# Performance work log

Measured on AMD Instinct MI355X. Metric: run time of the kernel, lower is better.

Reference implementation:

```python
import jax, jax.numpy as jnp
import numpy as np

B, N, D, DEPTH = 1, 512, 128, 4


def mlp_apply(W, x):
    # W: (depth, d, d), x: (..., d). First layer has no activation, then silu before each matmul.
    x = x @ W[0]
    for i in range(1, DEPTH):
        x = jax.nn.silu(x) @ W[i]
    return x


def _binop(x, y):
    # linear recurrence combine: s_t = a_t * s_{t-1} + b_t
    a1, b1 = x
    a2, b2 = y
    return (a1 * a2, a2 * b1 + b2)


def setup_inputs() -> dict:
    key = jax.random.key(0)
    ks = jax.random.split(key, 7)
    s = 0.02  # scale for projection weights (torch Linear-like init magnitude)
    return {
        "seq": jax.random.normal(ks[0], (B, N, D), jnp.float32),
        "W_mem": jax.random.normal(ks[1], (DEPTH, D, D), jnp.float32) * (D ** -0.5),
        "W_q": jax.random.normal(ks[2], (D, D), jnp.float32) * s,
        "W_kv": jax.random.normal(ks[3], (D, 2 * D), jnp.float32) * s,
        "W_mom": jax.random.normal(ks[4], (D, 1), jnp.float32) * s,
        "W_step": jax.random.normal(ks[5], (D, 1), jnp.float32) * s,
        "W_decay": jax.random.normal(ks[6], (D, 1), jnp.float32) * s,
    }


def reference(seq, W_mem, W_q, W_kv, W_mom, W_step, W_decay):
    b, n, d = seq.shape
    # --- store_memories ---
    adaptive_lr = (seq @ W_step)[..., 0]            # (b, n)
    adaptive_mom = seq @ W_mom                      # (b, n, 1)
    decay = jax.nn.sigmoid(seq @ W_decay)           # (b, n, 1)

    kv = seq.reshape(b * n, d) @ W_kv               # (bn, 2d)
    keys, values = kv[:, :d], kv[:, d:]

    def loss_fn(W, k, v):
        pred = mlp_apply(W, k)                      # (d,)
        # (pred - v)^2 .mean(-1).sum() for a single sample == mean over d
        return jnp.mean((pred - v) ** 2)

    # per-sample meta-gradients wrt memory MLP weights
    losses, grads = jax.vmap(jax.value_and_grad(loss_fn, argnums=0), in_axes=(None, 0, 0))(W_mem, keys, values)
    grads = grads.reshape(b, n, DEPTH, d, d)
    surprise = grads * (-adaptive_lr)[..., None, None, None]   # (b,n,depth,d,d)

    # momentum_t = adaptive_mom_t * momentum_{t-1} + surprise_t  (assoc. scan over n)
    am = adaptive_mom[..., None, None]              # (b, n, 1, 1, 1)
    _, momentum = jax.lax.associative_scan(_binop, (am, surprise), axis=1)

    # update_t = (1 - decay_t) * update_{t-1} + momentum_t
    dec = (1.0 - decay)[..., None, None]            # (b, n, 1, 1, 1)
    _, updates = jax.lax.associative_scan(_binop, (dec, momentum), axis=1)

    # --- retrieve_memories with per-token updated weights ---
    q = (seq @ W_q).reshape(b * n, d)
    W_tok = (W_mem[None, None] + updates).reshape(b * n, DEPTH, d, d)
    retrieved = jax.vmap(mlp_apply)(W_tok, q).reshape(b, n, d)
    return retrieved
```

## Files before the change

kernel.cpp:

```cpp
#include <hip/hip_runtime.h>
#include <hip/hip_bf16.h>
#include <math.h>

#define N 512
#define NN (N*N)
#define D 128
#define DD (D*D)
#define ND (N*D)
#define LSTR 132
#define CSTR 68

__device__ __forceinline__ float sigmoidf_(float x) { return 1.f / (1.f + expf(-x)); }

__global__ void k_transpose(const float* __restrict__ W_mem, float* __restrict__ WT) {
    int idx = blockIdx.x * 256 + threadIdx.x;
    int l = idx / DD;
    int r = idx % DD;
    int i = r / D;
    int j = r % D;
    WT[idx] = W_mem[(l + 1) * DD + j * D + i];
}

__global__ __launch_bounds__(512) void k_phase1(
    const float* __restrict__ seq, const float* __restrict__ W_mem,
    const float* __restrict__ W_q, const float* __restrict__ W_kv,
    const float* __restrict__ W_mom, const float* __restrict__ W_step,
    const float* __restrict__ W_decay, const float* __restrict__ WT,
    float* __restrict__ Q, float* __restrict__ INS, float* __restrict__ ES,
    float* __restrict__ am, float* __restrict__ dec)
{
    __shared__ float s_seq[D], s_v[D], s_cur[D];
    __shared__ float s_h[4][D];
    __shared__ float s_part[4][D];
    __shared__ float s_p3[4][3][D];
    __shared__ float s_red[8];
    __shared__ float s_lr;

    const int t = blockIdx.x;
    const int tid = threadIdx.x;
    const int j = tid & 127;
    const int p = tid >> 7;
    const int i0 = p * 32;

    if (p == 0) s_seq[j] = seq[t * D + j];
    __syncthreads();

    float ps = 0.f;
    if (p == 1) ps = s_seq[j] * W_step[j];
    else if (p == 2) ps = s_seq[j] * W_mom[j];
    else if (p == 3) ps = s_seq[j] * W_decay[j];
#pragma unroll
    for (int off = 32; off > 0; off >>= 1) ps += __shfl_down(ps, off);
    if ((tid & 63) == 0) s_red[tid >> 6] = ps;
    __syncthreads();
    if (tid == 0) s_lr = s_red[2] + s_red[3];
    else if (tid == 1) am[t] = s_red[4] + s_red[5];
    else if (tid == 2) dec[t] = 1.f - sigmoidf_(s_red[6] + s_red[7]);

    float kp = 0.f, vp = 0.f, qp = 0.f;
#pragma unroll 8
    for (int ii = 0; ii < 32; ii++) {
        int i = i0 + ii;
        float si = s_seq[i];
        kp += si * W_kv[i * 256 + j];
        vp += si * W_kv[i * 256 + 128 + j];
        qp += si * W_q[i * 128 + j];
    }
    s_p3[p][0][j] = kp; s_p3[p][1][j] = vp; s_p3[p][2][j] = qp;
    __syncthreads();
    if (p == 0) {
        float kj = s_p3[0][0][j] + s_p3[1][0][j] + s_p3[2][0][j] + s_p3[3][0][j];
        s_cur[j] = kj;
        INS[t * D + j] = kj;
    } else if (p == 1) {
        s_v[j] = s_p3[0][1][j] + s_p3[1][1][j] + s_p3[2][1][j] + s_p3[3][1][j];
    } else if (p == 2) {
        Q[t * D + j] = s_p3[0][2][j] + s_p3[1][2][j] + s_p3[2][2][j] + s_p3[3][2][j];
    }
    __syncthreads();

    for (int l = 0; l < 4; l++) {
        const float* Wl = W_mem + l * DD;
        float yp = 0.f;
#pragma unroll 8
        for (int ii = 0; ii < 32; ii++) {
            int i = i0 + ii;
            yp += s_cur[i] * Wl[i * D + j];
        }
        s_part[p][j] = yp;
        __syncthreads();
        if (p == 0) {
            float y = s_part[0][j] + s_part[1][j] + s_part[2][j] + s_part[3][j];
            s_h[l][j] = y;
            if (l < 3) {
                float a = y * sigmoidf_(y);
                s_cur[j] = a;
                INS[(l + 1) * ND + t * D + j] = a;
            }
        }
        __syncthreads();
    }

    if (p == 0) {
        float e = -s_lr * (2.f / (float)D) * (s_h[3][j] - s_v[j]);
        ES[3 * ND + t * D + j] = e;
        s_cur[j] = e;
    }
    __syncthreads();

    for (int l = 3; l >= 1; l--) {
        const float* Wt = WT + (l - 1) * DD;
        float gp = 0.f;
#pragma unroll 8
        for (int ii = 0; ii < 32; ii++) {
            int i = i0 + ii;
            gp += s_cur[i] * Wt[i * D + j];
        }
        s_part[p][j] = gp;
        __syncthreads();
        if (p == 0) {
            float g = s_part[0][j] + s_part[1][j] + s_part[2][j] + s_part[3][j];
            float h = s_h[l - 1][j];
            float sg = sigmoidf_(h);
            float e2 = g * (sg * (1.f + h * (1.f - sg)));
            ES[(l - 1) * ND + t * D + j] = e2;
            s_cur[j] = e2;
        }
        __syncthreads();
    }
}

__global__ __launch_bounds__(512) void k_logscan(
    const float* __restrict__ am, const float* __restrict__ dec,
    double* __restrict__ LA, double* __restrict__ LDp, int* __restrict__ NC)
{
    __shared__ double sa[N], sd[N];
    __shared__ int sn[N];
    const int t = threadIdx.x;
    float a = am[t];
    float d = dec[t];
    sa[t] = log((double)fmaxf(fabsf(a), 1e-38f));
    sd[t] = log((double)fmaxf(d, 1e-38f));
    sn[t] = (a < 0.f) ? 1 : 0;
    __syncthreads();
    for (int off = 1; off < N; off <<= 1) {
        double va = 0.0, vd = 0.0; int vn = 0;
        if (t >= off) { va = sa[t - off]; vd = sd[t - off]; vn = sn[t - off]; }
        __syncthreads();
        sa[t] += va; sd[t] += vd; sn[t] += vn;
        __syncthreads();
    }
    LA[t] = sa[t]; LDp[t] = sd[t]; NC[t] = sn[t];
}

__global__ __launch_bounds__(256) void k_build(
    const double* __restrict__ LA, const double* __restrict__ LDp,
    const int* __restrict__ NC,
    float* __restrict__ Amat, float* __restrict__ Dmat)
{
    int idx = blockIdx.x * 256 + threadIdx.x;
    int u = idx >> 9;
    int s = idx & (N - 1);
    float va = 0.f, vd = 0.f;
    if (s <= u) {
        va = expf((float)(LA[u] - LA[s]));
        if ((NC[u] - NC[s]) & 1) va = -va;
        vd = expf((float)(LDp[u] - LDp[s]));
    }
    Amat[idx] = va;
    Dmat[idx] = vd;
}

__global__ __launch_bounds__(256) void k_betamm(
    const float* __restrict__ Dmat, const float* __restrict__ Amat,
    float* __restrict__ betaP)
{
    const int bs = blockIdx.x;
    const int bt = blockIdx.y;
    const int z  = blockIdx.z;
    if (bs > bt) return;
    const int span = bt - bs + 1;
    const int chunk = (span + 3) >> 2;
    const int kBeg = bs + z * chunk;
    const int kEnd = (kBeg + chunk < bt + 1) ? (kBeg + chunk) : (bt + 1);
    if (kBeg >= kEnd) return;

    __shared__ float sA[32 * 34];
    __shared__ float sDT[32 * 34];

    const int tid = threadIdx.x;
    const int tx = tid & 15;
    const int ty = tid >> 4;
    float acc00 = 0.f, acc01 = 0.f, acc10 = 0.f, acc11 = 0.f;

    for (int kt = kBeg; kt < kEnd; kt++) {
        for (int i = tid; i < 1024; i += 256) {
            int r = i >> 5, c = i & 31;
            sA[r * 34 + c]  = Amat[(kt * 32 + r) * N + bs * 32 + c];
            sDT[c * 34 + r] = Dmat[(bt * 32 + r) * N + kt * 32 + c];
        }
        __syncthreads();
#pragma unroll 8
        for (int k = 0; k < 32; k++) {
            float2 a = *(float2*)&sA[k * 34 + 2 * tx];
            float2 d = *(float2*)&sDT[k * 34 + 2 * ty];
            acc00 += d.x * a.x; acc01 += d.x * a.y;
            acc10 += d.y * a.x; acc11 += d.y * a.y;
        }
        __syncthreads();
    }
    float* bp = betaP + z * NN + (bt * 32 + 2 * ty) * N + bs * 32 + 2 * tx;
    *(float2*)bp       = make_float2(acc00, acc01);
    *(float2*)(bp + N) = make_float2(acc10, acc11);
}

__global__ __launch_bounds__(256) void k_betared(
    const float* __restrict__ betaP, float* __restrict__ beta)
{
    int idx4 = blockIdx.x * 256 + threadIdx.x;
    int t  = idx4 >> 7;
    int s0 = (idx4 & 127) * 4;
    int bt = t >> 5, bs = s0 >> 5;
    float4 v = make_float4(0.f, 0.f, 0.f, 0.f);
    if (bs <= bt) {
        int span = bt - bs + 1;
        int chunk = (span + 3) >> 2;
        int nz = (span + chunk - 1) / chunk;
        v = *(const float4*)(betaP + t * N + s0);
        for (int z = 1; z < nz; z++) {
            float4 u = *(const float4*)(betaP + z * NN + t * N + s0);
            v.x += u.x; v.y += u.y; v.z += u.z; v.w += u.w;
        }
    }
    *(float4*)(beta + t * N + s0) = v;
}

__global__ __launch_bounds__(256) void k_layer(
    const float* __restrict__ Xsrc, float* __restrict__ Pout,
    const float* __restrict__ Wl, const float* __restrict__ INSl,
    const float* __restrict__ ESl, const float* __restrict__ beta,
    int mode)
{
    const int r = blockIdx.x;
    const int z = blockIdx.y;
    const bool isW = (z == 8);
    if (!isW && 4 * z > r) return;
    const int t0 = r * 16;
    const int lane = threadIdx.x;

    __shared__ __align__(16) float sX[16 * LSTR];
    __shared__ __align__(16) float sI[64 * LSTR];
    __shared__ __align__(16) float sE[32 * LSTR];
    __shared__ __align__(16) float sc[16 * CSTR];

    const int nzs = (r >> 2) + 1;
#pragma unroll
    for (int i = 0; i < 2; i++) {
        int f4 = lane + 256 * i;
        int row = f4 >> 5, c4 = f4 & 31;
        float4 v = ((const float4*)(Xsrc + t0 * D))[f4];
        if (mode) {
            for (int zz = 1; zz < nzs; zz++) {
                float4 u = ((const float4*)(Xsrc + zz * ND + t0 * D))[f4];
                v.x += u.x; v.y += u.y; v.z += u.z; v.w += u.w;
            }
            float4 w = ((const float4*)(Xsrc + 8 * ND + t0 * D))[f4];
            v.x += w.x; v.y += w.y; v.z += w.z; v.w += w.w;
            v.x = v.x * sigmoidf_(v.x); v.y = v.y * sigmoidf_(v.y);
            v.z = v.z * sigmoidf_(v.z); v.w = v.w * sigmoidf_(v.w);
        }
        *(float4*)(sX + row * LSTR + c4 * 4) = v;
    }

    if (isW) {
        __syncthreads();
        const int ti  = lane >> 4;
        const int j8  = (lane & 15) * 8;
        float acc[8];
#pragma unroll
        for (int b = 0; b < 8; b++) acc[b] = 0.f;
#pragma unroll 4
        for (int k = 0; k < D; k++) {
            float4 w0 = *(const float4*)(Wl + k * D + j8);
            float4 w1 = *(const float4*)(Wl + k * D + j8 + 4);
            float xv = sX[ti * LSTR + k];
            acc[0] += xv * w0.x; acc[1] += xv * w0.y;
            acc[2] += xv * w0.z; acc[3] += xv * w0.w;
            acc[4] += xv * w1.x; acc[5] += xv * w1.y;
            acc[6] += xv * w1.z; acc[7] += xv * w1.w;
        }
        float* yp = Pout + 8 * ND + (t0 + ti) * D + j8;
        *(float4*)yp       = make_float4(acc[0], acc[1], acc[2], acc[3]);
        *(float4*)(yp + 4) = make_float4(acc[4], acc[5], acc[6], acc[7]);
        return;
    }

    const int s0 = z * 64;

#pragma unroll
    for (int i = 0; i < 8; i++) {
        int f4 = lane + 256 * i;
        int row = f4 >> 5, c4 = f4 & 31;
        float4 a = ((const float4*)(INSl + s0 * D))[f4];
        *(float4*)(sI + row * LSTR + c4 * 4) = a;
    }

    const int rp = lane >> 5;
    const int sp = lane & 31;
    float b00 = beta[(t0 + 2 * rp) * N + s0 + sp];
    float b01 = beta[(t0 + 2 * rp) * N + s0 + sp + 32];
    float b10 = beta[(t0 + 2 * rp + 1) * N + s0 + sp];
    float b11 = beta[(t0 + 2 * rp + 1) * N + s0 + sp + 32];
    __syncthreads();

    float g00 = 0.f, g01 = 0.f, g10 = 0.f, g11 = 0.f;
#pragma unroll 8
    for (int k4 = 0; k4 < D; k4 += 4) {
        float4 a0 = *(float4*)(sX + (2 * rp) * LSTR + k4);
        float4 a1 = *(float4*)(sX + (2 * rp + 1) * LSTR + k4);
        float4 p0 = *(float4*)(sI + sp * LSTR + k4);
        float4 p1 = *(float4*)(sI + (sp + 32) * LSTR + k4);
        g00 += a0.x * p0.x + a0.y * p0.y + a0.z * p0.z + a0.w * p0.w;
        g01 += a0.x * p1.x + a0.y * p1.y + a0.z * p1.z + a0.w * p1.w;
        g10 += a1.x * p0.x + a1.y * p0.y + a1.z * p0.z + a1.w * p0.w;
        g11 += a1.x * p1.x + a1.y * p1.y + a1.z * p1.z + a1.w * p1.w;
    }
    sc[(2 * rp) * CSTR + sp]          = g00 * b00;
    sc[(2 * rp) * CSTR + sp + 32]     = g01 * b01;
    sc[(2 * rp + 1) * CSTR + sp]      = g10 * b10;
    sc[(2 * rp + 1) * CSTR + sp + 32] = g11 * b11;

    const int tp = lane >> 5;
    const int jc = (lane & 31) * 4;
    float acc[2][4];
#pragma unroll
    for (int a = 0; a < 2; a++)
#pragma unroll
        for (int b = 0; b < 4; b++) acc[a][b] = 0.f;

    for (int sub = 0; sub < 2; sub++) {
        __syncthreads();
#pragma unroll
        for (int i = 0; i < 4; i++) {
            int f4 = lane + 256 * i;
            int row = f4 >> 5, c4 = f4 & 31;
            float4 b = ((const float4*)(ESl + (s0 + sub * 32) * D))[f4];
            *(float4*)(sE + row * LSTR + c4 * 4) = b;
        }
        __syncthreads();
        const float* scp0 = sc + tp * CSTR + sub * 32;
        const float* scp1 = sc + (tp + 8) * CSTR + sub * 32;
#pragma unroll 8
        for (int s = 0; s < 32; s++) {
            float c0 = scp0[s];
            float c1 = scp1[s];
            float4 e = *(float4*)(sE + s * LSTR + jc);
            acc[0][0] += c0 * e.x; acc[0][1] += c0 * e.y;
            acc[0][2] += c0 * e.z; acc[0][3] += c0 * e.w;
            acc[1][0] += c1 * e.x; acc[1][1] += c1 * e.y;
            acc[1][2] += c1 * e.z; acc[1][3] += c1 * e.w;
        }
    }

    float* yp0 = Pout + z * ND + (t0 + tp) * D + jc;
    float* yp1 = Pout + z * ND + (t0 + tp + 8) * D + jc;
    *(float4*)yp0 = make_float4(acc[0][0], acc[0][1], acc[0][2], acc[0][3]);
    *(float4*)yp1 = make_float4(acc[1][0], acc[1][1], acc[1][2], acc[1][3]);
}

__global__ __launch_bounds__(256) void k_reduce(
    const float* __restrict__ P, float* __restrict__ out)
{
    int f4 = blockIdx.x * 256 + threadIdx.x;
    int t = f4 >> 5;
    int r = t >> 4;
    int nzs = (r >> 2) + 1;
    float4 v = ((const float4*)P)[f4];
    for (int zz = 1; zz < nzs; zz++) {
        float4 u = ((const float4*)(P + zz * ND))[f4];
        v.x += u.x; v.y += u.y; v.z += u.z; v.w += u.w;
    }
    float4 w = ((const float4*)(P + 8 * ND))[f4];
    v.x += w.x; v.y += w.y; v.z += w.z; v.w += w.w;
    ((float4*)out)[f4] = v;
}

extern "C" void kernel_launch(void* const* d_in, const int* in_sizes, int n_in,
                              void* d_out, int out_size, void* d_ws, size_t ws_size,
                              hipStream_t stream) {
    const float* seq     = (const float*)d_in[0];
    const float* W_mem   = (const float*)d_in[1];
    const float* W_q     = (const float*)d_in[2];
    const float* W_kv    = (const float*)d_in[3];
    const float* W_mom   = (const float*)d_in[4];
    const float* W_step  = (const float*)d_in[5];
    const float* W_decay = (const float*)d_in[6];
    float* out = (float*)d_out;

    float* ws   = (float*)d_ws;
    float* am   = ws;
    float* dec  = am + N;
    float* Q    = dec + N;
    float* INS  = Q + ND;
    float* ES   = INS + 4 * ND;
    float* beta = ES + 4 * ND;
    float* WT   = beta + NN;
    float* Amat = WT + 3 * DD;
    float* Dmat = Amat + NN;
    float* Pa   = Dmat + NN;
    float* Pb   = Pa + 9 * ND;
    double* LA  = (double*)(Pb + 9 * ND);
    double* LDp = LA + N;
    int* NC     = (int*)(LDp + N);
    float* betaP = Pa;

    k_transpose<<<192, 256, 0, stream>>>(W_mem, WT);
    k_phase1<<<N, 512, 0, stream>>>(seq, W_mem, W_q, W_kv, W_mom, W_step, W_decay,
                                    WT, Q, INS, ES, am, dec);
    k_logscan<<<1, N, 0, stream>>>(am, dec, LA, LDp, NC);
    k_build<<<(NN) / 256, 256, 0, stream>>>(LA, LDp, NC, Amat, Dmat);
    dim3 mmgrid(N / 32, N / 32, 4);
    k_betamm<<<mmgrid, 256, 0, stream>>>(Dmat, Amat, betaP);
    k_betared<<<NN / 4 / 256, 256, 0, stream>>>(betaP, beta);

    dim3 lgrid(32, 9);
    k_layer<<<lgrid, 256, 0, stream>>>(Q,  Pa, W_mem,          INS,          ES,          beta, 0);
    k_layer<<<lgrid, 256, 0, stream>>>(Pa, Pb, W_mem + DD,     INS + ND,     ES + ND,     beta, 1);
    k_layer<<<lgrid, 256, 0, stream>>>(Pb, Pa, W_mem + 2 * DD, INS + 2 * ND, ES + 2 * ND, beta, 1);
    k_layer<<<lgrid, 256, 0, stream>>>(Pa, Pb, W_mem + 3 * DD, INS + 3 * ND, ES + 3 * ND, beta, 1);
    k_reduce<<<64, 256, 0, stream>>>(Pb, out);
}
```

Measured before the change: 163.2 us.

## Process four tokens per block in phase1 with one token per 128-thread group

Restructures k_phase1 so each 512-thread block handles four tokens, with each 128-thread group owning one token and each thread computing a full 128-length dot product. This replaces the old split-K across four thread groups, dropping the shared-memory partial-sum reductions and the extra barriers. Hidden activations move into registers. In exchange each thread runs a longer serial loop, and the grid shrinks to 128 blocks, which may underfill the GPU's compute units, while loads of the shared weights are now shared by four tokens per block.

Result: slower. 172.5 us (+5.7%).

```diff
diff --git a/kernel.cpp b/kernel.cpp
--- a/kernel.cpp
+++ b/kernel.cpp
@@ -29,104 +29,111 @@
     float* __restrict__ Q, float* __restrict__ INS, float* __restrict__ ES,
     float* __restrict__ am, float* __restrict__ dec)
 {
-    __shared__ float s_seq[D], s_v[D], s_cur[D];
-    __shared__ float s_h[4][D];
-    __shared__ float s_part[4][D];
-    __shared__ float s_p3[4][3][D];
-    __shared__ float s_red[8];
-    __shared__ float s_lr;
-
-    const int t = blockIdx.x;
+    __shared__ float s_seq[4][D];
+    __shared__ float s_bufA[4][D];
+    __shared__ float s_bufB[4][D];
+    __shared__ float s_red[4][2][3];
+    __shared__ float s_lr[4];
+
     const int tid = threadIdx.x;
-    const int j = tid & 127;
-    const int p = tid >> 7;
-    const int i0 = p * 32;
-
-    if (p == 0) s_seq[j] = seq[t * D + j];
+    const int tok = tid >> 7;
+    const int j   = tid & 127;
+    const int t   = blockIdx.x * 4 + tok;
+
+    float sv = seq[t * D + j];
+    s_seq[tok][j] = sv;
+
+    float p0 = sv * W_step[j];
+    float p1 = sv * W_mom[j];
+    float p2 = sv * W_decay[j];
+#pragma unroll
+    for (int off = 32; off > 0; off >>= 1) {
+        p0 += __shfl_down(p0, off);
+        p1 += __shfl_down(p1, off);
+        p2 += __shfl_down(p2, off);
+    }
+    if ((tid & 63) == 0) {
+        int w = (tid >> 6) & 1;
+        s_red[tok][w][0] = p0;
+        s_red[tok][w][1] = p1;
+        s_red[tok][w][2] = p2;
+    }
     __syncthreads();
-
-    float ps = 0.f;
-    if (p == 1) ps = s_seq[j] * W_step[j];
-    else if (p == 2) ps = s_seq[j] * W_mom[j];
-    else if (p == 3) ps = s_seq[j] * W_decay[j];
-#pragma unroll
-    for (int off = 32; off > 0; off >>= 1) ps += __shfl_down(ps, off);
-    if ((tid & 63) == 0) s_red[tid >> 6] = ps;
+    if (j == 0) {
+        s_lr[tok] = s_red[tok][0][0] + s_red[tok][1][0];
+        am[t]     = s_red[tok][0][1] + s_red[tok][1][1];
+        dec[t]    = 1.f - sigmoidf_(s_red[tok][0][2] + s_red[tok][1][2]);
+    }
+
+    float kj = 0.f, vj = 0.f, qj = 0.f;
+    {
+        const float* sq = s_seq[tok];
+#pragma unroll 8
+        for (int i = 0; i < D; i++) {
+            float si = sq[i];
+            kj += si * W_kv[i * 256 + j];
+            vj += si * W_kv[i * 256 + 128 + j];
+            qj += si * W_q[i * 128 + j];
+        }
+    }
+    Q[t * D + j] = qj;
+    INS[t * D + j] = kj;
+    s_bufA[tok][j] = kj;
     __syncthreads();
-    if (tid == 0) s_lr = s_red[2] + s_red[3];
-    else if (tid == 1) am[t] = s_red[4] + s_red[5];
-    else if (tid == 2) dec[t] = 1.f - sigmoidf_(s_red[6] + s_red[7]);
-
-    float kp = 0.f, vp = 0.f, qp = 0.f;
-#pragma unroll 8
-    for (int ii = 0; ii < 32; ii++) {
-        int i = i0 + ii;
-        float si = s_seq[i];
-        kp += si * W_kv[i * 256 + j];
-        vp += si * W_kv[i * 256 + 128 + j];
-        qp += si * W_q[i * 128 + j];
-    }
-    s_p3[p][0][j] = kp; s_p3[p][1][j] = vp; s_p3[p][2][j] = qp;
-    __syncthreads();
-    if (p == 0) {
-        float kj = s_p3[0][0][j] + s_p3[1][0][j] + s_p3[2][0][j] + s_p3[3][0][j];
-        s_cur[j] = kj;
-        INS[t * D + j] = kj;
-    } else if (p == 1) {
-        s_v[j] = s_p3[0][1][j] + s_p3[1][1][j] + s_p3[2][1][j] + s_p3[3][1][j];
-    } else if (p == 2) {
-        Q[t * D + j] = s_p3[0][2][j] + s_p3[1][2][j] + s_p3[2][2][j] + s_p3[3][2][j];
-    }
-    __syncthreads();
-
-    for (int l = 0; l < 4; l++) {
-        const float* Wl = W_mem + l * DD;
-        float yp = 0.f;
-#pragma unroll 8
-        for (int ii = 0; ii < 32; ii++) {
-            int i = i0 + ii;
-            yp += s_cur[i] * Wl[i * D + j];
-        }
-        s_part[p][j] = yp;
-        __syncthreads();
-        if (p == 0) {
-            float y = s_part[0][j] + s_part[1][j] + s_part[2][j] + s_part[3][j];
-            s_h[l][j] = y;
+
+    float hreg[4];
+    float pred = 0.f;
+    {
+        float* curs[2] = { &s_bufA[0][0], &s_bufB[0][0] };
+        for (int l = 0; l < 4; l++) {
+            const float* cur = curs[l & 1] + tok * D;
+            float* nxt = curs[(l + 1) & 1] + tok * D;
+            const float* Wp = W_mem + l * DD + j;
+            float a0 = 0.f, a1 = 0.f, a2 = 0.f, a3 = 0.f;
+#pragma unroll 8
+            for (int i = 0; i < D; i += 4) {
+                a0 += cur[i]     * Wp[i * D];
+                a1 += cur[i + 1] * Wp[(i + 1) * D];
+                a2 += cur[i + 2] * Wp[(i + 2) * D];
+                a3 += cur[i + 3] * Wp[(i + 3) * D];
+            }
+            float y = (a0 + a1) + (a2 + a3);
+            hreg[l] = y;
             if (l < 3) {
                 float a = y * sigmoidf_(y);
-                s_cur[j] = a;
+                nxt[j] = a;
                 INS[(l + 1) * ND + t * D + j] = a;
+            } else {
+                pred = y;
             }
-        }
-        __syncthreads();
-    }
-
-    if (p == 0) {
-        float e = -s_lr * (2.f / (float)D) * (s_h[3][j] - s_v[j]);
+            __syncthreads();
+        }
+
+        float e = -s_lr[tok] * (2.f / (float)D) * (pred - vj);
         ES[3 * ND + t * D + j] = e;
-        s_cur[j] = e;
-    }
-    __syncthreads();
-
-    for (int l = 3; l >= 1; l--) {
-        const float* Wt = WT + (l - 1) * DD;
-        float gp = 0.f;
-#pragma unroll 8
-        for (int ii = 0; ii < 32; ii++) {
-            int i = i0 + ii;
-            gp += s_cur[i] * Wt[i * D + j];
-        }
-        s_part[p][j] = gp;
-        __syncthreads();
-        if (p == 0) {
-            float g = s_part[0][j] + s_part[1][j] + s_part[2][j] + s_part[3][j];
-            float h = s_h[l - 1][j];
+        curs[0][tok * D + j] = e;
+        __syncthreads();
+
+        for (int l = 3; l >= 1; l--) {
+            const float* cur = curs[(3 - l) & 1] + tok * D;
+            float* nxt = curs[(3 - l + 1) & 1] + tok * D;
+            const float* Wp = WT + (l - 1) * DD + j;
+            float a0 = 0.f, a1 = 0.f, a2 = 0.f, a3 = 0.f;
+#pragma unroll 8
+            for (int i = 0; i < D; i += 4) {
+                a0 += cur[i]     * Wp[i * D];
+                a1 += cur[i + 1] * Wp[(i + 1) * D];
+                a2 += cur[i + 2] * Wp[(i + 2) * D];
+                a3 += cur[i + 3] * Wp[(i + 3) * D];
+            }
+            float g = (a0 + a1) + (a2 + a3);
+            float h = hreg[l - 1];
             float sg = sigmoidf_(h);
             float e2 = g * (sg * (1.f + h * (1.f - sg)));
             ES[(l - 1) * ND + t * D + j] = e2;
-            s_cur[j] = e2;
-        }
-        __syncthreads();
+            nxt[j] = e2;
+            __syncthreads();
+        }
     }
 }
 
@@ -296,7 +303,6 @@
     }
 
     const int s0 = z * 64;
-
 #pragma unroll
     for (int i = 0; i < 8; i++) {
         int f4 = lane + 256 * i;
@@ -415,8 +421,8 @@
     float* betaP = Pa;
 
     k_transpose<<<192, 256, 0, stream>>>(W_mem, WT);
-    k_phase1<<<N, 512, 0, stream>>>(seq, W_mem, W_q, W_kv, W_mom, W_step, W_decay,
-                                    WT, Q, INS, ES, am, dec);
+    k_phase1<<<N / 4, 512, 0, stream>>>(seq, W_mem, W_q, W_kv, W_mom, W_step, W_decay,
+                                        WT, Q, INS, ES, am, dec);
     k_logscan<<<1, N, 0, stream>>>(am, dec, LA, LDp, NC);
     k_build<<<(NN) / 256, 256, 0, stream>>>(LA, LDp, NC, Amat, Dmat);
     dim3 mmgrid(N / 32, N / 32, 4);
```
